# Performance work log

Measured on AMD Instinct MI355X. Metric: run time of the kernel, lower is better.

## Reference

```python
import jax, jax.numpy as jnp
import numpy as np

H = 16  # n_heads


def setup_inputs() -> dict:
    key = jax.random.key(0)
    ks = jax.random.split(key, 8)
    N, L, dm = 4, 2048, 1024
    scale = 0.02
    rn = lambda k, shape: jax.random.normal(k, shape, dtype=jnp.float32)
    return {
        "queries": rn(ks[0], (N, L, dm)),
        "keys": rn(ks[1], (N, L, dm)),
        "values": rn(ks[2], (N, L, dm)),
        "Wq": rn(ks[3], (dm, dm)) * scale, "bq": jnp.zeros((dm,), jnp.float32),
        "Wk": rn(ks[4], (dm, dm)) * scale, "bk": jnp.zeros((dm,), jnp.float32),
        "Wv": rn(ks[5], (dm, dm)) * scale, "bv": jnp.zeros((dm,), jnp.float32),
        "Wo": rn(ks[6], (dm, dm)) * scale, "bo": jnp.zeros((dm,), jnp.float32),
    }


def _forward(queries, keys, values, Wq, bq, Wk, bk, Wv, bv, Wo, bo):
    N, L, _ = queries.shape
    q = (queries @ Wq + bq).reshape(N, L, H, -1)  # [N,L,H,D]
    k = (keys @ Wk + bk).reshape(N, L, H, -1)     # [N,L,H,D]
    v = (values @ Wv + bv).reshape(N, L, H, -1)   # [N,L,H,K]
    qp = jax.nn.elu(q) + 1.0
    kp = jax.nn.elu(k) + 1.0
    D = qp.shape[-1]
    K = v.shape[-1]

    # Causal linear attention: cumulative outer-product recurrence over time.
    def step(sums, inp):
        q_t, k_t, v_t = inp  # each [N,H,D] / [N,H,K]
        sums = sums + jnp.einsum('bhd,bhk->bhdk', k_t, v_t)
        out_t = jnp.einsum('bhdk,bhd->bhk', sums, q_t)
        return sums, out_t

    init = jnp.zeros((N, H, D, K), qp.dtype)
    xs = (jnp.swapaxes(qp, 0, 1), jnp.swapaxes(kp, 0, 1), jnp.swapaxes(v, 0, 1))
    _, res = jax.lax.scan(step, init, xs)  # [L,N,H,K]
    res = jnp.swapaxes(res, 0, 1)          # [N,L,H,K]
    # Original divides elementwise by cumsum of query features (D == K).
    Z = jnp.cumsum(qp, axis=1)             # [N,L,H,D]
    out = (res / Z).reshape(N, L, -1)
    return out @ Wo + bo


def reference(queries, keys, values, Wq, bq, Wk, bk, Wv, bv, Wo, bo):
    return _forward(queries, keys, values, Wq, bq, Wk, bk, Wv, bv, Wo, bo)
```

## Files before the change

kernel.cpp:

```cpp
#include <hip/hip_runtime.h>
#include <hip/hip_bf16.h>

typedef __hip_bfloat16 bf16;

#define N_B   4
#define LSEQ  2048
#define DM    1024
#define NH    16
#define HD    64
#define MROWS (N_B * LSEQ)
#define TCH   64
#define NC    (LSEQ / TCH)
#define PS    72

typedef short bf16x8 __attribute__((ext_vector_type(8)));
typedef float f32x4  __attribute__((ext_vector_type(4)));

__device__ __forceinline__ float u2f(unsigned short u){ return __uint_as_float(((unsigned)u) << 16); }
__device__ __forceinline__ unsigned short f2u(float x){
    bf16 h = __float2bfloat16(x);
    return *reinterpret_cast<unsigned short*>(&h);
}

__device__ __forceinline__ void g2l16(const void* g, void* l) {
    __builtin_amdgcn_global_load_lds(
        (const __attribute__((address_space(1))) unsigned int*)g,
        (__attribute__((address_space(3))) unsigned int*)l, 16, 0, 0);
}

__device__ __forceinline__ void tr4x4(const uint2 v[4], uint2 o[4]) {
    o[0].x = __builtin_amdgcn_perm(v[1].x, v[0].x, 0x05040100u);
    o[0].y = __builtin_amdgcn_perm(v[3].x, v[2].x, 0x05040100u);
    o[1].x = __builtin_amdgcn_perm(v[1].x, v[0].x, 0x07060302u);
    o[1].y = __builtin_amdgcn_perm(v[3].x, v[2].x, 0x07060302u);
    o[2].x = __builtin_amdgcn_perm(v[1].y, v[0].y, 0x05040100u);
    o[2].y = __builtin_amdgcn_perm(v[3].y, v[2].y, 0x05040100u);
    o[3].x = __builtin_amdgcn_perm(v[1].y, v[0].y, 0x07060302u);
    o[3].y = __builtin_amdgcn_perm(v[3].y, v[2].y, 0x07060302u);
}

__global__ __launch_bounds__(256) void cvt3_f32_bf16(
    const float* __restrict__ x0, const float* __restrict__ x1, const float* __restrict__ x2,
    bf16* __restrict__ y0, bf16* __restrict__ y1, bf16* __restrict__ y2, int per)
{
    int which = blockIdx.x / per;
    const float* x = (which == 0) ? x0 : (which == 1) ? x1 : x2;
    bf16* y = (which == 0) ? y0 : (which == 1) ? y1 : y2;
    int i = (blockIdx.x - which * per) * 256 + threadIdx.x;
    float4 v = ((const float4*)x)[i];
    ushort4 o = make_ushort4(f2u(v.x), f2u(v.y), f2u(v.z), f2u(v.w));
    ((ushort4*)y)[i] = o;
}

__global__ __launch_bounds__(256) void transpose_w4(
    const float* __restrict__ W0, const float* __restrict__ W1,
    const float* __restrict__ W2, const float* __restrict__ W3,
    bf16* __restrict__ T0, bf16* __restrict__ T1,
    bf16* __restrict__ T2, bf16* __restrict__ T3)
{
    const int z = blockIdx.z;
    const float* W = (z == 0) ? W0 : (z == 1) ? W1 : (z == 2) ? W2 : W3;
    bf16* Wt = (z == 0) ? T0 : (z == 1) ? T1 : (z == 2) ? T2 : T3;

    __shared__ unsigned short t[64][65];
    const int n0 = blockIdx.x * 64;
    const int k0 = blockIdx.y * 64;
    #pragma unroll
    for (int i = 0; i < 16; ++i) {
        int e = i * 256 + threadIdx.x;
        int r = e >> 6, c = e & 63;
        t[c][r] = f2u(W[(size_t)(k0 + r) * DM + n0 + c]);
    }
    __syncthreads();
    #pragma unroll
    for (int i = 0; i < 16; ++i) {
        int e = i * 256 + threadIdx.x;
        int r = e >> 6, c = e & 63;
        ((unsigned short*)Wt)[(size_t)(n0 + r) * DM + k0 + c] = t[r][c];
    }
}

template <typename TO, int MF>
__global__ __launch_bounds__(512, 2) void gemm_mfma3(
    const bf16* __restrict__ A0, const bf16* __restrict__ A1, const bf16* __restrict__ A2,
    const bf16* __restrict__ B0, const bf16* __restrict__ B1, const bf16* __restrict__ B2,
    const float* __restrict__ c0, const float* __restrict__ c1, const float* __restrict__ c2,
    TO* __restrict__ C0, TO* __restrict__ C1, TO* __restrict__ C2,
    int actMask, int M, int N, int K)
{
    constexpr int BM  = MF * 32;
    constexpr int MH  = MF / 2;
    constexpr int ASZ = MF * 16 * 64;
    constexpr int BSZ = 128 * 64;
    constexpr int LA  = MF / 4;
    constexpr int RSZ = 2 * ASZ + 2 * BSZ;

    const int z = blockIdx.z;
    const bf16* A  = (z == 0) ? A0 : (z == 1) ? A1 : A2;
    const bf16* Bt = (z == 0) ? B0 : (z == 1) ? B1 : B2;
    const float* bias = (z == 0) ? c0 : (z == 1) ? c1 : c2;
    TO* C = (z == 0) ? C0 : (z == 1) ? C1 : C2;
    const int act = (actMask >> z) & 1;

    __shared__ __align__(16) short smem[2 * RSZ];

    const int tid  = threadIdx.x;
    const int m0   = blockIdx.x * BM;
    const int n0   = blockIdx.y * 256;
    const int wave = tid >> 6;
    const int lane = tid & 63;
    const int wm   = wave >> 2;
    const int wn   = wave & 3;
    const int quad = lane >> 4;
    const int l16  = lane & 15;
    const int xsw  = l16 & 7;

    f32x4 acc[MF][4] = {};
    bf16x8 Areg[MH][2], Breg[4][2];

    const int NT = K >> 6;

    auto regA = [&](int buf, int h) -> short* { return smem + buf * RSZ + h * ASZ; };
    auto regB = [&](int buf, int h) -> short* { return smem + buf * RSZ + 2 * ASZ + h * BSZ; };

    auto stageA = [&](int t, int half, int buf) {
        short* dst = regA(buf, half);
        #pragma unroll
        for (int i = 0; i < LA; ++i) {
            int e = i * 512 + tid;
            int r = e >> 3;
            int col = ((e & 7) ^ (r & 7)) * 8;
            int grow = m0 + half * (MH * 16) + (r >> (MH == 4 ? 6 : 5)) * (MF * 16)
                       + (r & (MH * 16 - 1));
            g2l16(A + (size_t)grow * K + t * 64 + col, dst + e * 8);
        }
    };
    auto stageB = [&](int t, int half, int buf) {
        short* dst = regB(buf, half);
        #pragma unroll
        for (int i = 0; i < 2; ++i) {
            int e = i * 512 + tid;
            int r = e >> 3;
            int col = ((e & 7) ^ (r & 7)) * 8;
            int grow = n0 + ((r >> 5) << 6) + half * 32 + (r & 31);
            g2l16(Bt + (size_t)grow * K + t * 64 + col, dst + e * 8);
        }
    };

    auto ldA = [&](const short* base, int m2, int ks) -> bf16x8 {
        int row  = wm * (MH * 16) + m2 * 16 + l16;
        int slot = (ks * 4 + quad) ^ xsw;
        return *(const bf16x8*)(base + row * 64 + slot * 8);
    };
    auto ldB = [&](const short* base, int n2, int ks) -> bf16x8 {
        int row  = wn * 32 + n2 * 16 + l16;
        int slot = (ks * 4 + quad) ^ xsw;
        return *(const bf16x8*)(base + row * 64 + slot * 8);
    };

    stageA(0, 0, 0); stageB(0, 0, 0); stageB(0, 1, 0); stageA(0, 1, 0);
    stageA(1, 0, 1); stageB(1, 0, 1);
    if constexpr (MF == 8) asm volatile("s_waitcnt vmcnt(4)");
    else                   asm volatile("s_waitcnt vmcnt(3)");
    __builtin_amdgcn_s_barrier();

    for (int T = 0; T < NT; ++T) {
        const int bT = T & 1;
        const short* Ab0 = regA(bT, 0);
        const short* Ab1 = regA(bT, 1);
        const short* Bb0 = regB(bT, 0);
        const short* Bb1 = regB(bT, 1);

        #pragma unroll
        for (int m2 = 0; m2 < MH; ++m2) {
            Areg[m2][0] = ldA(Ab0, m2, 0);
            Areg[m2][1] = ldA(Ab0, m2, 1);
        }
        #pragma unroll
        for (int n2 = 0; n2 < 2; ++n2) {
            Breg[n2][0] = ldB(Bb0, n2, 0);
            Breg[n2][1] = ldB(Bb0, n2, 1);
        }
        if (T + 1 < NT) stageB(T + 1, 1, (T + 1) & 1);
        __builtin_amdgcn_s_barrier();
        asm volatile("s_waitcnt lgkmcnt(0)");
        __builtin_amdgcn_s_setprio(1);
        #pragma unroll
        for (int m2 = 0; m2 < MH; ++m2)
            #pragma unroll
            for (int n2 = 0; n2 < 2; ++n2) {
                acc[m2][n2] = __builtin_amdgcn_mfma_f32_16x16x32_bf16(
                    Areg[m2][0], Breg[n2][0], acc[m2][n2], 0, 0, 0);
                acc[m2][n2] = __builtin_amdgcn_mfma_f32_16x16x32_bf16(
                    Areg[m2][1], Breg[n2][1], acc[m2][n2], 0, 0, 0);
            }
        __builtin_amdgcn_s_setprio(0);
        __builtin_amdgcn_s_barrier();

        #pragma unroll
        for (int n2 = 0; n2 < 2; ++n2) {
            Breg[2 + n2][0] = ldB(Bb1, n2, 0);
            Breg[2 + n2][1] = ldB(Bb1, n2, 1);
        }
        if (T + 1 < NT) stageA(T + 1, 1, (T + 1) & 1);
        __builtin_amdgcn_s_barrier();
        asm volatile("s_waitcnt lgkmcnt(0)");
        __builtin_amdgcn_s_setprio(1);
        #pragma unroll
        for (int m2 = 0; m2 < MH; ++m2)
            #pragma unroll
            for (int n2 = 0; n2 < 2; ++n2) {
                acc[m2][2 + n2] = __builtin_amdgcn_mfma_f32_16x16x32_bf16(
                    Areg[m2][0], Breg[2 + n2][0], acc[m2][2 + n2], 0, 0, 0);
                acc[m2][2 + n2] = __builtin_amdgcn_mfma_f32_16x16x32_bf16(
                    Areg[m2][1], Breg[2 + n2][1], acc[m2][2 + n2], 0, 0, 0);
            }
        __builtin_amdgcn_s_setprio(0);
        __builtin_amdgcn_s_barrier();

        #pragma unroll
        for (int m2 = 0; m2 < MH; ++m2) {
            Areg[m2][0] = ldA(Ab1, m2, 0);
            Areg[m2][1] = ldA(Ab1, m2, 1);
        }
        if (T + 2 < NT) stageA(T + 2, 0, bT);
        __builtin_amdgcn_s_barrier();
        asm volatile("s_waitcnt lgkmcnt(0)");
        __builtin_amdgcn_s_setprio(1);
        #pragma unroll
        for (int m2 = 0; m2 < MH; ++m2)
            #pragma unroll
            for (int n2 = 0; n2 < 2; ++n2) {
                acc[MH + m2][n2] = __builtin_amdgcn_mfma_f32_16x16x32_bf16(
                    Areg[m2][0], Breg[n2][0], acc[MH + m2][n2], 0, 0, 0);
                acc[MH + m2][n2] = __builtin_amdgcn_mfma_f32_16x16x32_bf16(
                    Areg[m2][1], Breg[n2][1], acc[MH + m2][n2], 0, 0, 0);
            }
        __builtin_amdgcn_s_setprio(0);
        __builtin_amdgcn_s_barrier();

        if (T + 2 < NT) stageB(T + 2, 0, bT);
        __builtin_amdgcn_s_barrier();
        asm volatile("s_waitcnt lgkmcnt(0)");
        __builtin_amdgcn_s_setprio(1);
        #pragma unroll
        for (int m2 = 0; m2 < MH; ++m2)
            #pragma unroll
            for (int n2 = 0; n2 < 2; ++n2) {
                acc[MH + m2][2 + n2] = __builtin_amdgcn_mfma_f32_16x16x32_bf16(
                    Areg[m2][0], Breg[2 + n2][0], acc[MH + m2][2 + n2], 0, 0, 0);
                acc[MH + m2][2 + n2] = __builtin_amdgcn_mfma_f32_16x16x32_bf16(
                    Areg[m2][1], Breg[2 + n2][1], acc[MH + m2][2 + n2], 0, 0, 0);
            }
        __builtin_amdgcn_s_setprio(0);
        if (T < NT - 2) {
            if constexpr (MF == 8) asm volatile("s_waitcnt vmcnt(4)");
            else                   asm volatile("s_waitcnt vmcnt(3)");
        } else {
            asm volatile("s_waitcnt vmcnt(0)");
        }
        __builtin_amdgcn_s_barrier();
    }

    #pragma unroll
    for (int ni = 0; ni < 4; ++ni) {
        int col = n0 + wn * 64 + ni * 16 + l16;
        float bv = bias[col];
        #pragma unroll
        for (int mi = 0; mi < MF; ++mi) {
            #pragma unroll
            for (int r = 0; r < 4; ++r) {
                int row = m0 + wm * (MF * 16) + mi * 16 + quad * 4 + r;
                float x = acc[mi][ni][r] + bv;
                if (act) x = (x > 0.f) ? (x + 1.f) : __expf(x);
                if constexpr (sizeof(TO) == 2)
                    ((bf16*)C)[(size_t)row * N + col] = __float2bfloat16(x);
                else
                    ((float*)C)[(size_t)row * N + col] = x;
            }
        }
    }
}

__global__ __launch_bounds__(256) void chunk_state(
    const bf16* __restrict__ qp, const bf16* __restrict__ kp,
    const bf16* __restrict__ v,
    bf16* __restrict__ chunkSB, float* __restrict__ chunkZ)
{
    __shared__ __align__(16) unsigned short kpT_s[64 * PS];
    __shared__ __align__(16) unsigned short vT_s [64 * PS];
    __shared__ __align__(16) unsigned short qp_s [64 * PS];
    __shared__ float red[4][64];

    const int bh = blockIdx.x;
    const int c  = blockIdx.y;
    const int n  = bh >> 4, h = bh & 15;
    const int tid = threadIdx.x;
    const size_t rowbase = (size_t)n * LSEQ + (size_t)c * TCH;

    {
        const int t4 = tid >> 4;
        const int c0 = (tid & 15) * 4;
        uint2 ku[4], vu[4], qu[4];
        #pragma unroll
        for (int j = 0; j < 4; ++j) {
            size_t g = (rowbase + t4 * 4 + j) * DM + h * HD + c0;
            ku[j] = *(const uint2*)((const unsigned short*)kp + g);
            vu[j] = *(const uint2*)((const unsigned short*)v  + g);
            qu[j] = *(const uint2*)((const unsigned short*)qp + g);
        }
        #pragma unroll
        for (int j = 0; j < 4; ++j)
            *(uint2*)&qp_s[(t4 * 4 + j) * PS + c0] = qu[j];
        uint2 kc[4], vc[4];
        tr4x4(ku, kc);
        tr4x4(vu, vc);
        #pragma unroll
        for (int i = 0; i < 4; ++i) {
            *(uint2*)&kpT_s[(c0 + i) * PS + t4 * 4] = kc[i];
            *(uint2*)&vT_s [(c0 + i) * PS + t4 * 4] = vc[i];
        }
    }
    __syncthreads();

    const int wave = tid >> 6, lane = tid & 63;
    const int quad = lane >> 4, l16 = lane & 15;

    f32x4 acc[4] = {};
    #pragma unroll
    for (int kk = 0; kk < 2; ++kk) {
        bf16x8 af = *(const bf16x8*)&kpT_s[(wave*16 + l16) * PS + kk*32 + quad*8];
        #pragma unroll
        for (int ni = 0; ni < 4; ++ni) {
            bf16x8 bfr = *(const bf16x8*)&vT_s[(ni*16 + l16) * PS + kk*32 + quad*8];
            acc[ni] = __builtin_amdgcn_mfma_f32_16x16x32_bf16(af, bfr, acc[ni], 0, 0, 0);
        }
    }
    unsigned short* Sout = (unsigned short*)chunkSB + (((size_t)bh * NC + c) << 12);
    #pragma unroll
    for (int ni = 0; ni < 4; ++ni) {
        int k = ni*16 + l16;
        #pragma unroll
        for (int r = 0; r < 4; ++r) {
            int d = wave*16 + quad*4 + r;
            Sout[d * 64 + k] = f2u(acc[ni][r]);
        }
    }

    {
        int d = tid & 63, part = tid >> 6;
        float s = 0.f;
        #pragma unroll
        for (int t = part*16; t < part*16 + 16; ++t)
            s += u2f(qp_s[t * PS + d]);
        red[part][d] = s;
    }
    __syncthreads();
    if (tid < 64)
        chunkZ[((size_t)bh * NC + c) * 64 + tid] =
            red[0][tid] + red[1][tid] + red[2][tid] + red[3][tid];
}

__global__ __launch_bounds__(256) void prefix_state(
    const bf16* __restrict__ chunkSB, bf16* __restrict__ SpB,
    float* __restrict__ chunkZ)
{
    const int bh = blockIdx.x;
    const int elem = blockIdx.y * 256 + threadIdx.x;
    const unsigned short* p = (const unsigned short*)chunkSB + (((size_t)bh * NC) << 12) + elem;
    unsigned short* o = (unsigned short*)SpB + (((size_t)bh * NC) << 12) + elem;
    float run = 0.f;
    #pragma unroll
    for (int c = 0; c < NC; ++c) {
        float x = u2f(p[(size_t)c << 12]);
        o[(size_t)c << 12] = f2u(run);
        run += x;
    }
    if (blockIdx.y == 0 && threadIdx.x < 64) {
        float* pz = chunkZ + (size_t)bh * NC * 64 + threadIdx.x;
        float rz = 0.f;
        for (int c = 0; c < NC; ++c) {
            float x = pz[c * 64];
            pz[c * 64] = rz;
            rz += x;
        }
    }
}

__global__ __launch_bounds__(256) void chunk_attn(
    const bf16* __restrict__ qp, const bf16* __restrict__ kp,
    const bf16* __restrict__ v, const bf16* __restrict__ SpB,
    const float* __restrict__ chunkZ, bf16* __restrict__ att)
{
    __shared__ __align__(16) unsigned short qp_s [64 * PS];
    __shared__ __align__(16) unsigned short kp_s [64 * PS];
    __shared__ __align__(16) unsigned short SpT_s[64 * PS];
    __shared__ __align__(16) unsigned short vT_s [64 * PS];
    __shared__ __align__(16) unsigned short qpT_s[64 * PS];
    unsigned short* P_s = qp_s;

    const int bh = blockIdx.x;
    const int c  = blockIdx.y;
    const int n  = bh >> 4, h = bh & 15;
    const int tid = threadIdx.x;
    const size_t rowbase = (size_t)n * LSEQ + (size_t)c * TCH;
    const unsigned short* Spb = (const unsigned short*)SpB + (((size_t)bh * NC + c) << 12);

    {
        const int t4 = tid >> 4;
        const int c0 = (tid & 15) * 4;
        uint2 qu[4], ku[4], vu[4], su[4];
        #pragma unroll
        for (int j = 0; j < 4; ++j) {
            size_t g = (rowbase + t4 * 4 + j) * DM + h * HD + c0;
            qu[j] = *(const uint2*)((const unsigned short*)qp + g);
            ku[j] = *(const uint2*)((const unsigned short*)kp + g);
            vu[j] = *(const uint2*)((const unsigned short*)v  + g);
            su[j] = *(const uint2*)(Spb + (t4 * 4 + j) * 64 + c0);
        }
        #pragma unroll
        for (int j = 0; j < 4; ++j) {
            *(uint2*)&qp_s[(t4 * 4 + j) * PS + c0] = qu[j];
            *(uint2*)&kp_s[(t4 * 4 + j) * PS + c0] = ku[j];
        }
        uint2 vc[4], qc[4], sc[4];
        tr4x4(vu, vc);
        tr4x4(qu, qc);
        tr4x4(su, sc);
        #pragma unroll
        for (int i = 0; i < 4; ++i) {
            *(uint2*)&vT_s [(c0 + i) * PS + t4 * 4] = vc[i];
            *(uint2*)&qpT_s[(c0 + i) * PS + t4 * 4] = qc[i];
            *(uint2*)&SpT_s[(c0 + i) * PS + t4 * 4] = sc[i];
        }
    }
    __syncthreads();

    const int wave = tid >> 6, lane = tid & 63;
    const int quad = lane >> 4, l16 = lane & 15;
    const int mrow = wave * 16;

    f32x4 acc[4]  = {};
    f32x4 zacc[4] = {};
    f32x4 pacc[4] = {};

    const unsigned short ONE = 0x3F80;

    #pragma unroll
    for (int kk = 0; kk < 2; ++kk) {
        bf16x8 af = *(const bf16x8*)&qp_s[(mrow + l16) * PS + kk*32 + quad*8];
        bf16x8 tf;
        #pragma unroll
        for (int j = 0; j < 8; ++j) {
            int s = kk*32 + quad*8 + j;
            tf[j] = (short)((s <= mrow + l16) ? ONE : 0);
        }
        #pragma unroll
        for (int ni = 0; ni < 4; ++ni) {
            int boff = (ni*16 + l16) * PS + kk*32 + quad*8;
            bf16x8 b_sp = *(const bf16x8*)&SpT_s[boff];
            bf16x8 b_kp = *(const bf16x8*)&kp_s [boff];
            bf16x8 b_qt = *(const bf16x8*)&qpT_s[boff];
            acc [ni] = __builtin_amdgcn_mfma_f32_16x16x32_bf16(af, b_sp, acc [ni], 0, 0, 0);
            pacc[ni] = __builtin_amdgcn_mfma_f32_16x16x32_bf16(af, b_kp, pacc[ni], 0, 0, 0);
            zacc[ni] = __builtin_amdgcn_mfma_f32_16x16x32_bf16(tf, b_qt, zacc[ni], 0, 0, 0);
        }
    }

    __syncthreads();

    #pragma unroll
    for (int ni = 0; ni < 4; ++ni) {
        int s = ni*16 + l16;
        #pragma unroll
        for (int r = 0; r < 4; ++r) {
            int t = mrow + quad*4 + r;
            float pv = (s <= t) ? pacc[ni][r] : 0.f;
            P_s[t * PS + s] = f2u(pv);
        }
    }
    __syncthreads();

    #pragma unroll
    for (int kk = 0; kk < 2; ++kk) {
        bf16x8 af = *(const bf16x8*)&P_s[(mrow + l16) * PS + kk*32 + quad*8];
        #pragma unroll
        for (int ni = 0; ni < 4; ++ni) {
            bf16x8 b_v = *(const bf16x8*)&vT_s[(ni*16 + l16) * PS + kk*32 + quad*8];
            acc[ni] = __builtin_amdgcn_mfma_f32_16x16x32_bf16(af, b_v, acc[ni], 0, 0, 0);
        }
    }

    #pragma unroll
    for (int ni = 0; ni < 4; ++ni) {
        int k = ni*16 + l16;
        float zp = chunkZ[((size_t)bh * NC + c) * 64 + k];
        #pragma unroll
        for (int r = 0; r < 4; ++r) {
            int t = mrow + quad*4 + r;
            float o = acc[ni][r] / (zp + zacc[ni][r]);
            ((unsigned short*)att)[(rowbase + t) * DM + h * HD + k] = f2u(o);
        }
    }
}

extern "C" void kernel_launch(void* const* d_in, const int* in_sizes, int n_in,
                              void* d_out, int out_size, void* d_ws, size_t ws_size,
                              hipStream_t stream)
{
    const float* queries = (const float*)d_in[0];
    const float* keys    = (const float*)d_in[1];
    const float* values  = (const float*)d_in[2];
    const float* Wq = (const float*)d_in[3];
    const float* bq = (const float*)d_in[4];
    const float* Wk = (const float*)d_in[5];
    const float* bk = (const float*)d_in[6];
    const float* Wv = (const float*)d_in[7];
    const float* bv = (const float*)d_in[8];
    const float* Wo = (const float*)d_in[9];
    const float* bo = (const float*)d_in[10];
    float* out = (float*)d_out;

    char* w = (char*)d_ws;
    const size_t E2 = (size_t)MROWS * DM * 2;
    const size_t WB = (size_t)DM * DM * 2;
    bf16* qb  = (bf16*)(w + 0 * E2);
    bf16* kb  = (bf16*)(w + 1 * E2);
    bf16* vb  = (bf16*)(w + 2 * E2);
    bf16* Wqt = (bf16*)(w + 3 * E2 + 0 * WB);
    bf16* Wkt = (bf16*)(w + 3 * E2 + 1 * WB);
    bf16* Wvt = (bf16*)(w + 3 * E2 + 2 * WB);
    bf16* Wot = (bf16*)(w + 3 * E2 + 3 * WB);
    bf16* qp  = (bf16*)(w + 3 * E2 + 4 * WB);
    bf16* kp  = (bf16*)(w + 4 * E2 + 4 * WB);
    bf16* vv  = (bf16*)(w + 5 * E2 + 4 * WB);
    bf16* SpB = (bf16*)(w + 6 * E2 + 4 * WB);
    bf16*  chunkSB = kb;
    float* chunkZ  = (float*)Wqt;
    bf16*  att     = qb;

    const int n4 = (MROWS * DM) / 4;
    const int per = n4 / 256;
    cvt3_f32_bf16<<<3 * per, 256, 0, stream>>>(queries, keys, values, qb, kb, vb, per);

    transpose_w4<<<dim3(DM / 64, DM / 64, 4), 256, 0, stream>>>(
        Wq, Wk, Wv, Wo, Wqt, Wkt, Wvt, Wot);

    gemm_mfma3<bf16, 8><<<dim3(MROWS / 256, DM / 256, 3), 512, 0, stream>>>(
        qb, kb, vb, Wqt, Wkt, Wvt, bq, bk, bv, qp, kp, vv,
        0b011, MROWS, DM, DM);

    chunk_state <<<dim3(64, NC), 256, 0, stream>>>(qp, kp, vv, chunkSB, chunkZ);
    prefix_state<<<dim3(64, 16), 256, 0, stream>>>(chunkSB, SpB, chunkZ);
    chunk_attn  <<<dim3(64, NC), 256, 0, stream>>>(qp, kp, vv, SpB, chunkZ, att);

    gemm_mfma3<float, 4><<<dim3(MROWS / 128, DM / 256, 1), 512, 0, stream>>>(
        att, att, att, Wot, Wot, Wot, bo, bo, bo, out, out, out,
        0, MROWS, DM, DM);
}
```

Before: 301.7 us.

## Use K=32 tiles in projection GEMM for higher occupancy, fuse prep kernels

The QKV projection GEMM now uses a K-step of 32 instead of 64. That halves its LDS footprint (64 KB) so four 512-thread blocks per CU are allowed by the launch bounds, at the cost of twice as many pipeline iterations and barriers. The fp32-to-bf16 conversion and weight-transpose kernels are merged into one launch to save a kernel launch. The output GEMM becomes a dedicated non-templated kernel with no activation branch. The 256x256 tile with 128 fp32 accumulators per thread at four blocks per CU risks register spilling.

```diff
diff --git a/kernel.cpp b/kernel.cpp
--- a/kernel.cpp
+++ b/kernel.cpp
@@ -39,32 +39,33 @@
     o[3].y = __builtin_amdgcn_perm(v[3].y, v[2].y, 0x07060302u);
 }
 
-__global__ __launch_bounds__(256) void cvt3_f32_bf16(
+__global__ __launch_bounds__(256) void cvt_and_wt(
     const float* __restrict__ x0, const float* __restrict__ x1, const float* __restrict__ x2,
-    bf16* __restrict__ y0, bf16* __restrict__ y1, bf16* __restrict__ y2, int per)
-{
-    int which = blockIdx.x / per;
-    const float* x = (which == 0) ? x0 : (which == 1) ? x1 : x2;
-    bf16* y = (which == 0) ? y0 : (which == 1) ? y1 : y2;
-    int i = (blockIdx.x - which * per) * 256 + threadIdx.x;
-    float4 v = ((const float4*)x)[i];
-    ushort4 o = make_ushort4(f2u(v.x), f2u(v.y), f2u(v.z), f2u(v.w));
-    ((ushort4*)y)[i] = o;
-}
-
-__global__ __launch_bounds__(256) void transpose_w4(
+    bf16* __restrict__ y0, bf16* __restrict__ y1, bf16* __restrict__ y2,
     const float* __restrict__ W0, const float* __restrict__ W1,
     const float* __restrict__ W2, const float* __restrict__ W3,
     bf16* __restrict__ T0, bf16* __restrict__ T1,
-    bf16* __restrict__ T2, bf16* __restrict__ T3)
+    bf16* __restrict__ T2, bf16* __restrict__ T3, int per)
 {
-    const int z = blockIdx.z;
+    __shared__ unsigned short t[64][65];
+    const int bx = blockIdx.x;
+    if (bx < 3 * per) {
+        int which = bx / per;
+        const float* x = (which == 0) ? x0 : (which == 1) ? x1 : x2;
+        bf16* y = (which == 0) ? y0 : (which == 1) ? y1 : y2;
+        int i = (bx - which * per) * 256 + threadIdx.x;
+        float4 v = ((const float4*)x)[i];
+        ushort4 o = make_ushort4(f2u(v.x), f2u(v.y), f2u(v.z), f2u(v.w));
+        ((ushort4*)y)[i] = o;
+        return;
+    }
+    const int tt = bx - 3 * per;
+    const int z = tt >> 8;
+    const int rem = tt & 255;
     const float* W = (z == 0) ? W0 : (z == 1) ? W1 : (z == 2) ? W2 : W3;
     bf16* Wt = (z == 0) ? T0 : (z == 1) ? T1 : (z == 2) ? T2 : T3;
-
-    __shared__ unsigned short t[64][65];
-    const int n0 = blockIdx.x * 64;
-    const int k0 = blockIdx.y * 64;
+    const int n0 = (rem & 15) * 64;
+    const int k0 = (rem >> 4) * 64;
     #pragma unroll
     for (int i = 0; i < 16; ++i) {
         int e = i * 256 + threadIdx.x;
@@ -80,32 +81,174 @@
     }
 }
 
-template <typename TO, int MF>
-__global__ __launch_bounds__(512, 2) void gemm_mfma3(
+__global__ __launch_bounds__(512, 4) void gemm_proj_bk32(
     const bf16* __restrict__ A0, const bf16* __restrict__ A1, const bf16* __restrict__ A2,
     const bf16* __restrict__ B0, const bf16* __restrict__ B1, const bf16* __restrict__ B2,
     const float* __restrict__ c0, const float* __restrict__ c1, const float* __restrict__ c2,
-    TO* __restrict__ C0, TO* __restrict__ C1, TO* __restrict__ C2,
+    bf16* __restrict__ C0, bf16* __restrict__ C1, bf16* __restrict__ C2,
     int actMask, int M, int N, int K)
 {
-    constexpr int BM  = MF * 32;
-    constexpr int MH  = MF / 2;
-    constexpr int ASZ = MF * 16 * 64;
-    constexpr int BSZ = 128 * 64;
-    constexpr int LA  = MF / 4;
-    constexpr int RSZ = 2 * ASZ + 2 * BSZ;
-
     const int z = blockIdx.z;
     const bf16* A  = (z == 0) ? A0 : (z == 1) ? A1 : A2;
     const bf16* Bt = (z == 0) ? B0 : (z == 1) ? B1 : B2;
     const float* bias = (z == 0) ? c0 : (z == 1) ? c1 : c2;
-    TO* C = (z == 0) ? C0 : (z == 1) ? C1 : C2;
+    bf16* C = (z == 0) ? C0 : (z == 1) ? C1 : C2;
     const int act = (actMask >> z) & 1;
 
+    __shared__ __align__(16) short smem[2 * 16384];
+
+    const int tid  = threadIdx.x;
+    const int m0   = blockIdx.x * 256;
+    const int n0   = blockIdx.y * 256;
+    const int wave = tid >> 6;
+    const int lane = tid & 63;
+    const int wm   = wave >> 2;
+    const int wn   = wave & 3;
+    const int quad = lane >> 4;
+    const int l16  = lane & 15;
+    const int xsw  = (l16 >> 2) & 3;
+
+    f32x4 acc[8][4] = {};
+    bf16x8 Areg[4], Breg[4];
+
+    const int NT = K >> 5;
+
+    auto regA = [&](int buf, int h) -> short* { return smem + buf * 16384 + h * 4096; };
+    auto regB = [&](int buf, int h) -> short* { return smem + buf * 16384 + 8192 + h * 4096; };
+
+    auto stageA = [&](int t, int half, int buf) {
+        short* dst = regA(buf, half);
+        int e = tid, r = e >> 2;
+        int col = ((e & 3) ^ ((r >> 2) & 3)) * 8;
+        int grow = m0 + half * 64 + ((r >> 6) << 7) + (r & 63);
+        g2l16(A + (size_t)grow * K + t * 32 + col, dst + e * 8);
+    };
+    auto stageB = [&](int t, int half, int buf) {
+        short* dst = regB(buf, half);
+        int e = tid, r = e >> 2;
+        int col = ((e & 3) ^ ((r >> 2) & 3)) * 8;
+        int grow = n0 + ((r >> 5) << 6) + half * 32 + (r & 31);
+        g2l16(Bt + (size_t)grow * K + t * 32 + col, dst + e * 8);
+    };
+
+    auto ldA = [&](const short* base, int m2) -> bf16x8 {
+        int row  = wm * 64 + m2 * 16 + l16;
+        int slot = quad ^ xsw;
+        return *(const bf16x8*)(base + row * 32 + slot * 8);
+    };
+    auto ldB = [&](const short* base, int n2) -> bf16x8 {
+        int row  = wn * 32 + n2 * 16 + l16;
+        int slot = quad ^ xsw;
+        return *(const bf16x8*)(base + row * 32 + slot * 8);
+    };
+
+    stageA(0, 0, 0); stageB(0, 0, 0); stageB(0, 1, 0); stageA(0, 1, 0);
+    stageA(1, 0, 1); stageB(1, 0, 1);
+    asm volatile("s_waitcnt vmcnt(2)");
+    __builtin_amdgcn_s_barrier();
+
+    for (int T = 0; T < NT; ++T) {
+        const int bT = T & 1;
+        const short* Ab0 = regA(bT, 0);
+        const short* Ab1 = regA(bT, 1);
+        const short* Bb0 = regB(bT, 0);
+        const short* Bb1 = regB(bT, 1);
+
+        #pragma unroll
+        for (int m2 = 0; m2 < 4; ++m2) Areg[m2] = ldA(Ab0, m2);
+        #pragma unroll
+        for (int n2 = 0; n2 < 2; ++n2) Breg[n2] = ldB(Bb0, n2);
+        if (T + 1 < NT) stageB(T + 1, 1, (T + 1) & 1);
+        __builtin_amdgcn_s_barrier();
+        asm volatile("s_waitcnt lgkmcnt(0)");
+        __builtin_amdgcn_s_setprio(1);
+        #pragma unroll
+        for (int m2 = 0; m2 < 4; ++m2)
+            #pragma unroll
+            for (int n2 = 0; n2 < 2; ++n2)
+                acc[m2][n2] = __builtin_amdgcn_mfma_f32_16x16x32_bf16(
+                    Areg[m2], Breg[n2], acc[m2][n2], 0, 0, 0);
+        __builtin_amdgcn_s_setprio(0);
+        __builtin_amdgcn_s_barrier();
+
+        #pragma unroll
+        for (int n2 = 0; n2 < 2; ++n2) Breg[2 + n2] = ldB(Bb1, n2);
+        if (T + 1 < NT) stageA(T + 1, 1, (T + 1) & 1);
+        __builtin_amdgcn_s_barrier();
+        asm volatile("s_waitcnt lgkmcnt(0)");
+        __builtin_amdgcn_s_setprio(1);
+        #pragma unroll
+        for (int m2 = 0; m2 < 4; ++m2)
+            #pragma unroll
+            for (int n2 = 0; n2 < 2; ++n2)
+                acc[m2][2 + n2] = __builtin_amdgcn_mfma_f32_16x16x32_bf16(
+                    Areg[m2], Breg[2 + n2], acc[m2][2 + n2], 0, 0, 0);
+        __builtin_amdgcn_s_setprio(0);
+        __builtin_amdgcn_s_barrier();
+
+        #pragma unroll
+        for (int m2 = 0; m2 < 4; ++m2) Areg[m2] = ldA(Ab1, m2);
+        if (T + 2 < NT) stageA(T + 2, 0, bT);
+        __builtin_amdgcn_s_barrier();
+        asm volatile("s_waitcnt lgkmcnt(0)");
+        __builtin_amdgcn_s_setprio(1);
+        #pragma unroll
+        for (int m2 = 0; m2 < 4; ++m2)
+            #pragma unroll
+            for (int n2 = 0; n2 < 2; ++n2)
+                acc[4 + m2][n2] = __builtin_amdgcn_mfma_f32_16x16x32_bf16(
+                    Areg[m2], Breg[n2], acc[4 + m2][n2], 0, 0, 0);
+        __builtin_amdgcn_s_setprio(0);
+        __builtin_amdgcn_s_barrier();
+
+        if (T + 2 < NT) stageB(T + 2, 0, bT);
+        __builtin_amdgcn_s_barrier();
+        asm volatile("s_waitcnt lgkmcnt(0)");
+        __builtin_amdgcn_s_setprio(1);
+        #pragma unroll
+        for (int m2 = 0; m2 < 4; ++m2)
+            #pragma unroll
+            for (int n2 = 0; n2 < 2; ++n2)
+                acc[4 + m2][2 + n2] = __builtin_amdgcn_mfma_f32_16x16x32_bf16(
+                    Areg[m2], Breg[2 + n2], acc[4 + m2][2 + n2], 0, 0, 0);
+        __builtin_amdgcn_s_setprio(0);
+        if (T < NT - 2) asm volatile("s_waitcnt vmcnt(2)");
+        else            asm volatile("s_waitcnt vmcnt(0)");
+        __builtin_amdgcn_s_barrier();
+    }
+
+    #pragma unroll
+    for (int ni = 0; ni < 4; ++ni) {
+        int col = n0 + wn * 64 + ni * 16 + l16;
+        float bv = bias[col];
+        #pragma unroll
+        for (int mi = 0; mi < 8; ++mi) {
+            #pragma unroll
+            for (int r = 0; r < 4; ++r) {
+                int row = m0 + wm * 128 + mi * 16 + quad * 4 + r;
+                float x = acc[mi][ni][r] + bv;
+                if (act) x = (x > 0.f) ? (x + 1.f) : __expf(x);
+                ((unsigned short*)C)[(size_t)row * N + col] = f2u(x);
+            }
+        }
+    }
+}
+
+__global__ __launch_bounds__(512, 2) void gemm_out(
+    const bf16* __restrict__ A, const bf16* __restrict__ Bt,
+    const float* __restrict__ bias, float* __restrict__ C,
+    int M, int N, int K)
+{
+    constexpr int MF  = 4;
+    constexpr int MH  = MF / 2;
+    constexpr int ASZ = MF * 16 * 64;
+    constexpr int BSZ = 128 * 64;
+    constexpr int RSZ = 2 * ASZ + 2 * BSZ;
+
     __shared__ __align__(16) short smem[2 * RSZ];
 
     const int tid  = threadIdx.x;
-    const int m0   = blockIdx.x * BM;
+    const int m0   = blockIdx.x * (MF * 32);
     const int n0   = blockIdx.y * 256;
     const int wave = tid >> 6;
     const int lane = tid & 63;
@@ -125,15 +268,13 @@
 
     auto stageA = [&](int t, int half, int buf) {
         short* dst = regA(buf, half);
-        #pragma unroll
-        for (int i = 0; i < LA; ++i) {
-            int e = i * 512 + tid;
-            int r = e >> 3;
-            int col = ((e & 7) ^ (r & 7)) * 8;
-            int grow = m0 + half * (MH * 16) + (r >> (MH == 4 ? 6 : 5)) * (MF * 16)
-                       + (r & (MH * 16 - 1));
-            g2l16(A + (size_t)grow * K + t * 64 + col, dst + e * 8);
-        }
+        int e = tid;
+        if (e < 512) {
+        }
+        int r = e >> 3;
+        int col = ((e & 7) ^ (r & 7)) * 8;
+        int grow = m0 + half * (MH * 16) + ((r >> 5) << 6) + (r & (MH * 16 - 1));
+        g2l16(A + (size_t)grow * K + t * 64 + col, dst + e * 8);
     };
     auto stageB = [&](int t, int half, int buf) {
         short* dst = regB(buf, half);
@@ -160,8 +301,7 @@
 
     stageA(0, 0, 0); stageB(0, 0, 0); stageB(0, 1, 0); stageA(0, 1, 0);
     stageA(1, 0, 1); stageB(1, 0, 1);
-    if constexpr (MF == 8) asm volatile("s_waitcnt vmcnt(4)");
-    else                   asm volatile("s_waitcnt vmcnt(3)");
+    asm volatile("s_waitcnt vmcnt(3)");
     __builtin_amdgcn_s_barrier();
 
     for (int T = 0; T < NT; ++T) {
@@ -253,12 +393,8 @@
                     Areg[m2][1], Breg[2 + n2][1], acc[MH + m2][2 + n2], 0, 0, 0);
             }
         __builtin_amdgcn_s_setprio(0);
-        if (T < NT - 2) {
-            if constexpr (MF == 8) asm volatile("s_waitcnt vmcnt(4)");
-            else                   asm volatile("s_waitcnt vmcnt(3)");
-        } else {
-            asm volatile("s_waitcnt vmcnt(0)");
-        }
+        if (T < NT - 2) asm volatile("s_waitcnt vmcnt(3)");
+        else            asm volatile("s_waitcnt vmcnt(0)");
         __builtin_amdgcn_s_barrier();
     }
 
@@ -271,12 +407,7 @@
             #pragma unroll
             for (int r = 0; r < 4; ++r) {
                 int row = m0 + wm * (MF * 16) + mi * 16 + quad * 4 + r;
-                float x = acc[mi][ni][r] + bv;
-                if (act) x = (x > 0.f) ? (x + 1.f) : __expf(x);
-                if constexpr (sizeof(TO) == 2)
-                    ((bf16*)C)[(size_t)row * N + col] = __float2bfloat16(x);
-                else
-                    ((float*)C)[(size_t)row * N + col] = x;
+                C[(size_t)row * N + col] = acc[mi][ni][r] + bv;
             }
         }
     }
@@ -539,14 +670,12 @@
     float* chunkZ  = (float*)Wqt;
     bf16*  att     = qb;
 
-    const int n4 = (MROWS * DM) / 4;
-    const int per = n4 / 256;
-    cvt3_f32_bf16<<<3 * per, 256, 0, stream>>>(queries, keys, values, qb, kb, vb, per);
-
-    transpose_w4<<<dim3(DM / 64, DM / 64, 4), 256, 0, stream>>>(
-        Wq, Wk, Wv, Wo, Wqt, Wkt, Wvt, Wot);
-
-    gemm_mfma3<bf16, 8><<<dim3(MROWS / 256, DM / 256, 3), 512, 0, stream>>>(
+    const int per = (MROWS * DM) / 4 / 256;
+    cvt_and_wt<<<3 * per + 1024, 256, 0, stream>>>(
+        queries, keys, values, qb, kb, vb,
+        Wq, Wk, Wv, Wo, Wqt, Wkt, Wvt, Wot, per);
+
+    gemm_proj_bk32<<<dim3(MROWS / 256, DM / 256, 3), 512, 0, stream>>>(
         qb, kb, vb, Wqt, Wkt, Wvt, bq, bk, bv, qp, kp, vv,
         0b011, MROWS, DM, DM);
 
@@ -554,7 +683,6 @@
     prefix_state<<<dim3(64, 16), 256, 0, stream>>>(chunkSB, SpB, chunkZ);
     chunk_attn  <<<dim3(64, NC), 256, 0, stream>>>(qp, kp, vv, SpB, chunkZ, att);
 
-    gemm_mfma3<float, 4><<<dim3(MROWS / 128, DM / 256, 1), 512, 0, stream>>>(
-        att, att, att, Wot, Wot, Wot, bo, bo, bo, out, out, out,
-        0, MROWS, DM, DM);
-}
+    gemm_out<<<dim3(MROWS / 128, DM / 256, 1), 512, 0, stream>>>(
+        att, Wot, bo, out, MROWS, DM, DM);
+}
```

Result: slower. 708.5 us (+134.9%).
